# Optimization experiments

Hardware: AMD Instinct MI355X
Metric: run time of the kernel (lower is better)

The kernel has to match this reference:

```python
import jax, jax.numpy as jnp
import numpy as np

FRAME_RATE = 2048
B, T, L = 64, 256, 65536


def setup_inputs() -> dict:
    key = jax.random.key(0)
    ks = jax.random.split(key, 20)
    F = FRAME_RATE
    s = 0.05
    return {
        "alpha": jnp.sort(jax.random.randint(ks[0], (B, T), 0, L), axis=1).astype(jnp.int32),
        "sound": jax.random.normal(ks[1], (B, L), jnp.float32),
        "conv1_w": jax.random.normal(ks[2], (F - 2,), jnp.float32) * s,
        "conv1_b": jax.random.normal(ks[3], (1,), jnp.float32) * s,
        "conv2_w": jax.random.normal(ks[4], (32, 1, 3), jnp.float32) * s,
        "conv2_b": jax.random.normal(ks[5], (32,), jnp.float32) * s,
        "conv3_w": jax.random.normal(ks[6], (128, 32, 3), jnp.float32) * s,
        "conv3_b": jax.random.normal(ks[7], (128,), jnp.float32) * s,
        "lin_w": jax.random.normal(ks[8], (256, 129), jnp.float32) * s,
        "lin_b": jax.random.normal(ks[9], (256,), jnp.float32) * s,
        "w_ih": jax.random.normal(ks[10], (1024, 256), jnp.float32) * s,
        "w_hh": jax.random.normal(ks[11], (1024, 256), jnp.float32) * s,
        "b_ih": jax.random.normal(ks[12], (1024,), jnp.float32) * s,
        "b_hh": jax.random.normal(ks[13], (1024,), jnp.float32) * s,
        "out1_w": jax.random.normal(ks[14], (32, 256), jnp.float32) * s,
        "out1_b": jax.random.normal(ks[15], (32,), jnp.float32) * s,
        "out2_w": jax.random.normal(ks[16], (1, 32), jnp.float32) * s,
        "out2_b": jax.random.normal(ks[17], (1,), jnp.float32) * s,
    }


def reference(alpha, sound, conv1_w, conv1_b, conv2_w, conv2_b, conv3_w, conv3_b,
              lin_w, lin_b, w_ih, w_hh, b_ih, b_hh, out1_w, out1_b, out2_w, out2_b):
    F = conv1_w.shape[0] + 2  # frame_rate
    Bsz, Tlen = alpha.shape
    pad = F // 2
    # Vectorized gather of all per-timestep fragments (replaces nested python loops).
    padded = jnp.pad(sound, ((0, 0), (pad, pad)))               # [B, L + 2*(F//2)]
    idx = alpha[:, :, None] + jnp.arange(F)[None, None, :]      # [B, T, F]
    frags = jnp.take_along_axis(padded[:, None, :], idx, axis=2)  # [B, T, F]
    frags = frags.transpose(1, 0, 2)                            # [T, B, F]
    K = F - 2
    # conv1: 1->1 channel, kernel F-2, output length 3 (three big dot products)
    y1 = jnp.stack([jnp.einsum('tbf,f->tb', frags[:, :, i:i + K], conv1_w)
                    for i in range(3)], axis=-1) + conv1_b[0]   # [T, B, 3]
    # conv2: 1->32 channels, kernel 3, padding 1 (output length stays 3), then ReLU
    y1p = jnp.pad(y1, ((0, 0), (0, 0), (1, 1)))
    win = jnp.stack([y1p[:, :, l:l + 3] for l in range(3)], axis=2)  # [T, B, 3(l), 3(k)]
    y2 = jax.nn.relu(jnp.einsum('tblk,ck->tbcl', win, conv2_w[:, 0, :])
                     + conv2_b[None, None, :, None])            # [T, B, 32, 3]
    # conv3: 32->128 channels, kernel 3, no padding -> output length 1 (no relu, matching source)
    y3 = jnp.einsum('tbck,ock->tbo', y2, conv3_w) + conv3_b     # [T, B, 128]
    # interval = alpha_t - alpha_{t-1} (0 at t=0)
    prev = jnp.concatenate([jnp.zeros((Bsz, 1), alpha.dtype), alpha[:, :-1]], axis=1)
    interval = (alpha - prev).T.astype(frags.dtype)             # [T, B]
    x = jnp.concatenate([interval[..., None], y3], axis=-1)     # [T, B, 129]
    x = x @ lin_w.T + lin_b                                     # [T, B, 256]
    H = w_hh.shape[1]

    def step(carry, xt):
        h, c = carry
        g = xt @ w_ih.T + b_ih + h @ w_hh.T + b_hh              # [B, 4H]
        i_, f_, g_, o_ = jnp.split(g, 4, axis=-1)
        c = jax.nn.sigmoid(f_) * c + jax.nn.sigmoid(i_) * jnp.tanh(g_)
        h = jax.nn.sigmoid(o_) * jnp.tanh(c)
        return (h, c), None

    h0 = jnp.zeros((Bsz, H), x.dtype)
    (h, c), _ = jax.lax.scan(step, (h0, h0), x)
    ht = h[None]                                                # [1, B, 256]
    out = jax.nn.sigmoid(jax.nn.relu(ht @ out1_w.T + out1_b) @ out2_w.T + out2_b)
    return out                                                  # [1, B, 1]
```

## Files before the change

kernel.cpp:

```cpp
#include <hip/hip_runtime.h>
#include <math.h>

#define BSZ 64
#define TLEN 256
#define LSND 65536
#define ZSLOTS 144

__device__ __forceinline__ float sigm(float x) { return 1.f / (1.f + __expf(-x)); }
__device__ __forceinline__ float tanh_f(float x) {
  float e = __expf(-2.f * fabsf(x));
  return copysignf((1.f - e) / (1.f + e), x);
}
__device__ __forceinline__ int zslot(int k) { return (k / 33) * 36 + (k % 33); }

__global__ __launch_bounds__(256) void prep_kernel(
    const float* __restrict__ w_ih, const float* __restrict__ lin_w,
    const float* __restrict__ lin_b, const float* __restrict__ b_ih,
    const float* __restrict__ b_hh, float* __restrict__ Wc, float* __restrict__ bc)
{
  __shared__ float sRow[256];
  const int n = blockIdx.x;
  const int j = threadIdx.x;
  sRow[j] = w_ih[n * 256 + j];
  __syncthreads();
  if (j < 132) {
    float acc = 0.f;
    if (j < 129) {
      for (int k = 0; k < 256; ++k) acc += sRow[k] * lin_w[k * 129 + j];
    }
    Wc[n * 132 + j] = acc;
  } else if (j == 255) {
    float acc = b_ih[n] + b_hh[n];
    for (int k = 0; k < 256; ++k) acc += sRow[k] * lin_b[k];
    bc[n] = acc;
  }
}

__global__ __launch_bounds__(256) void transpose_w3(const float* __restrict__ w3,
                                                    float* __restrict__ w3t)
{
  int i = blockIdx.x * 256 + threadIdx.x;
  if (i < 96 * 128) { int s = i >> 7, o = i & 127; w3t[i] = w3[o * 96 + s]; }
}

__global__ __launch_bounds__(64) void conv_kernel(
    const int* __restrict__ alpha, const float* __restrict__ sound,
    const float* __restrict__ w1, const float* __restrict__ b1v,
    const float* __restrict__ w2, const float* __restrict__ b2,
    const float* __restrict__ w3t, const float* __restrict__ b3,
    float* __restrict__ z)
{
  __shared__ float win[2048];
  __shared__ float sY2[96];
  const int l = threadIdx.x;
  const int b = blockIdx.x >> 8;
  const int t = blockIdx.x & 255;
  const int a = alpha[b * TLEN + t];
  const int a0 = a - 1024;
  const float* srow = sound + (size_t)b * LSND;
  for (int x = l; x < 2048; x += 64) {
    int p = a0 + x;
    win[x] = (p >= 0 && p < LSND) ? srow[p] : 0.f;
  }
  __syncthreads();
  float acc0 = 0.f, acc1 = 0.f, acc2 = 0.f;
  for (int f = l; f < 2046; f += 64) {
    float wv = w1[f];
    acc0 += win[f] * wv;
    acc1 += win[f + 1] * wv;
    acc2 += win[f + 2] * wv;
  }
  for (int m = 32; m; m >>= 1) {
    acc0 += __shfl_xor(acc0, m);
    acc1 += __shfl_xor(acc1, m);
    acc2 += __shfl_xor(acc2, m);
  }
  const float bb = b1v[0];
  const float y11 = acc0 + bb, y12 = acc1 + bb, y13 = acc2 + bb;
  {
    int s = l;
    int c = s / 3, lp = s - c * 3;
    float wA = w2[c * 3], wB = w2[c * 3 + 1], wC = w2[c * 3 + 2];
    float v = (lp == 0) ? (y11 * wB + y12 * wC)
            : (lp == 1) ? (y11 * wA + y12 * wB + y13 * wC)
                        : (y12 * wA + y13 * wB);
    sY2[s] = fmaxf(v + b2[c], 0.f);
    if (l < 32) {
      s = 64 + l; c = s / 3; lp = s - c * 3;
      wA = w2[c * 3]; wB = w2[c * 3 + 1]; wC = w2[c * 3 + 2];
      v = (lp == 0) ? (y11 * wB + y12 * wC)
        : (lp == 1) ? (y11 * wA + y12 * wB + y13 * wC)
                    : (y12 * wA + y13 * wB);
      sY2[s] = fmaxf(v + b2[c], 0.f);
    }
  }
  __syncthreads();
  float o0 = b3[l], o1 = b3[l + 64];
  for (int s = 0; s < 96; ++s) {
    float yv = sY2[s];
    o0 += yv * w3t[s * 128 + l];
    o1 += yv * w3t[s * 128 + l + 64];
  }
  float* zrow = z + ((size_t)t * BSZ + b) * ZSLOTS;
  zrow[zslot(1 + l)] = o0;
  zrow[zslot(65 + l)] = o1;
  if (l == 0) {
    int prev = (t > 0) ? alpha[b * TLEN + t - 1] : 0;
    zrow[0] = (float)(a - prev);
  }
  if (l < 15) {
    int s = (l < 9) ? ((l / 3) * 36 + 33 + (l % 3)) : (138 + (l - 9));
    zrow[s] = 0.f;
  }
}

__global__ void __launch_bounds__(256, 1) lstm_kernel(
    const float* __restrict__ z, const float* __restrict__ Wc,
    const float* __restrict__ bc, const float* __restrict__ w_hh,
    unsigned long long* __restrict__ hbuf, float* __restrict__ hfin)
{
  __shared__ float sH[4][408];
  __shared__ float sP[64][20];
  __shared__ float sG[256];
  __shared__ float sBC[64];

  const int tid = threadIdx.x;
  const int btile = (int)blockIdx.x >> 4;
  const int jt    = (int)blockIdx.x & 15;
  const int w  = tid >> 6;
  const int nl = tid & 63;
  const int ng = ((nl >> 4) << 8) + (jt << 4) + (nl & 15);

  float4 wh[16];
  #pragma unroll
  for (int i = 0; i < 16; ++i)
    wh[i] = *(const float4*)&w_hh[ng * 256 + (w << 6) + (i << 2)];
  float4 wz[9];
  #pragma unroll
  for (int i = 0; i < 9; ++i) {
    float c0 = (i * 4 + 0 < 33) ? Wc[ng * 132 + w * 33 + i * 4 + 0] : 0.f;
    float c1 = (i * 4 + 1 < 33) ? Wc[ng * 132 + w * 33 + i * 4 + 1] : 0.f;
    float c2 = (i * 4 + 2 < 33) ? Wc[ng * 132 + w * 33 + i * 4 + 2] : 0.f;
    float c3 = (i * 4 + 3 < 33) ? Wc[ng * 132 + w * 33 + i * 4 + 3] : 0.f;
    wz[i] = make_float4(c0, c1, c2, c3);
  }
  if (tid < 64) sBC[tid] = bc[((tid >> 4) << 8) + (jt << 4) + (tid & 15)];

  const int zb = (tid < 144) ? tid / 36 : 0;
  const int zc4 = (tid < 144) ? (tid - zb * 36) << 2 : 0;
  float4 zpre = make_float4(0.f, 0.f, 0.f, 0.f);
  if (tid < 144) {
    *(float4*)&sH[zb][256 + zc4] =
        *(const float4*)&z[((size_t)0 * BSZ + (btile << 2) + zb) * ZSLOTS + zc4];
    zpre = *(const float4*)&z[((size_t)1 * BSZ + (btile << 2) + zb) * ZSLOTS + zc4];
  }
  float c_reg = 0.f;
  __syncthreads();

  const int pb = tid & 3;
  const int pjp = (tid & 63) >> 2;
  const int pbase = ((((btile << 2) + pb) << 8) | (w << 6) | pjp);

  for (int t = 0; t < TLEN; ++t) {
    {
      const unsigned long long* hsrc = hbuf + ((size_t)(t & 1) << 14);
      const unsigned tagw = (unsigned)t;
      int rem = 15;
      while (rem) {
        #pragma unroll
        for (int s = 0; s < 4; ++s) {
          if (rem & (1 << s)) {
            unsigned long long v = __hip_atomic_load(hsrc + pbase + (s << 4),
                __ATOMIC_RELAXED, __HIP_MEMORY_SCOPE_AGENT);
            if ((unsigned)v == tagw) {
              sH[pb][(w << 6) | (pjp + (s << 4))] = __uint_as_float((unsigned)(v >> 32));
              rem &= ~(1 << s);
            }
          }
        }
      }
    }
    float a0 = 0.f, a1 = 0.f, a2 = 0.f, a3 = 0.f;
    const int hb = w << 6;
    #pragma unroll
    for (int i = 0; i < 16; ++i) {
      const float4 wv = wh[i];
      float4 h;
      h = *(const float4*)&sH[0][hb + (i << 2)]; a0 += wv.x*h.x + wv.y*h.y + wv.z*h.z + wv.w*h.w;
      h = *(const float4*)&sH[1][hb + (i << 2)]; a1 += wv.x*h.x + wv.y*h.y + wv.z*h.z + wv.w*h.w;
      h = *(const float4*)&sH[2][hb + (i << 2)]; a2 += wv.x*h.x + wv.y*h.y + wv.z*h.z + wv.w*h.w;
      h = *(const float4*)&sH[3][hb + (i << 2)]; a3 += wv.x*h.x + wv.y*h.y + wv.z*h.z + wv.w*h.w;
    }
    const int zbase = 256 + w * 36;
    #pragma unroll
    for (int i = 0; i < 9; ++i) {
      const float4 wv = wz[i];
      float4 v;
      v = *(const float4*)&sH[0][zbase + (i << 2)]; a0 += wv.x*v.x + wv.y*v.y + wv.z*v.z + wv.w*v.w;
      v = *(const float4*)&sH[1][zbase + (i << 2)]; a1 += wv.x*v.x + wv.y*v.y + wv.z*v.z + wv.w*v.w;
      v = *(const float4*)&sH[2][zbase + (i << 2)]; a2 += wv.x*v.x + wv.y*v.y + wv.z*v.z + wv.w*v.w;
      v = *(const float4*)&sH[3][zbase + (i << 2)]; a3 += wv.x*v.x + wv.y*v.y + wv.z*v.z + wv.w*v.w;
    }
    sP[nl][0 + w] = a0;
    sP[nl][4 + w] = a1;
    sP[nl][8 + w] = a2;
    sP[nl][12 + w] = a3;
    __syncthreads();
    {
      const int rn = tid >> 2, rb = tid & 3;
      const float4 p = *(const float4*)&sP[rn][rb << 2];
      sG[tid] = p.x + p.y + p.z + p.w + sBC[rn];
    }
    if (t + 1 < TLEN && tid < 144)
      *(float4*)&sH[zb][256 + zc4] = zpre;
    __syncthreads();
    if (tid < 64) {
      float gi = sG[tid];
      float gf = sG[64 + tid];
      float gg = sG[128 + tid];
      float go = sG[192 + tid];
      c_reg = sigm(gf) * c_reg + sigm(gi) * tanh_f(gg);
      float hv = sigm(go) * tanh_f(c_reg);
      const int jl = tid >> 2, bb = tid & 3;
      const int widx = ((((btile << 2) + bb) << 8) | ((jt << 4) + jl));
      unsigned long long pk =
          ((unsigned long long)__float_as_uint(hv) << 32) | (unsigned)(t + 1);
      __hip_atomic_store(hbuf + (((size_t)((t + 1) & 1)) << 14) + widx, pk,
                         __ATOMIC_RELAXED, __HIP_MEMORY_SCOPE_AGENT);
      if (t == TLEN - 1) hfin[widx] = hv;
    }
    if (t + 2 < TLEN && tid < 144)
      zpre = *(const float4*)&z[((size_t)(t + 2) * BSZ + (btile << 2) + zb) * ZSLOTS + zc4];
  }
}

__global__ __launch_bounds__(256) void head_kernel(
    const float* __restrict__ hfin, const float* __restrict__ o1w,
    const float* __restrict__ o1b, const float* __restrict__ o2w,
    const float* __restrict__ o2b, float* __restrict__ out)
{
  __shared__ float sR[32];
  const int b = blockIdx.x;
  const int tid = threadIdx.x;
  const int m = tid >> 3, g = tid & 7;
  const float* h = hfin + b * 256;
  float acc = 0.f;
  for (int k = g * 32; k < g * 32 + 32; ++k) acc += h[k] * o1w[m * 256 + k];
  acc += __shfl_xor(acc, 1); acc += __shfl_xor(acc, 2); acc += __shfl_xor(acc, 4);
  if (g == 0) sR[m] = fmaxf(acc + o1b[m], 0.f);
  __syncthreads();
  if (tid == 0) {
    float s = o2b[0];
    for (int mm = 0; mm < 32; ++mm) s += sR[mm] * o2w[mm];
    out[b] = sigm(s);
  }
}

extern "C" void kernel_launch(void* const* d_in, const int* in_sizes, int n_in,
                              void* d_out, int out_size, void* d_ws, size_t ws_size,
                              hipStream_t stream) {
  (void)in_sizes; (void)n_in; (void)out_size; (void)ws_size;
  const int*   alpha = (const int*)  d_in[0];
  const float* sound = (const float*)d_in[1];
  const float* w1    = (const float*)d_in[2];
  const float* b1    = (const float*)d_in[3];
  const float* w2    = (const float*)d_in[4];
  const float* b2    = (const float*)d_in[5];
  const float* w3    = (const float*)d_in[6];
  const float* b3    = (const float*)d_in[7];
  const float* linw  = (const float*)d_in[8];
  const float* linb  = (const float*)d_in[9];
  const float* wih   = (const float*)d_in[10];
  const float* whh   = (const float*)d_in[11];
  const float* bih   = (const float*)d_in[12];
  const float* bhh   = (const float*)d_in[13];
  const float* o1w   = (const float*)d_in[14];
  const float* o1b   = (const float*)d_in[15];
  const float* o2w   = (const float*)d_in[16];
  const float* o2b   = (const float*)d_in[17];

  float* z    = (float*)d_ws;
  float* Wc   = z + 2359296;
  float* bc   = Wc + 135168;
  float* w3t  = bc + 1024;
  float* hfin = w3t + 12288;
  unsigned long long* hbuf =
      (unsigned long long*)(hfin + 16384);

  hipMemsetAsync(hbuf, 0, 32768 * 8, stream);

  prep_kernel<<<1024, 256, 0, stream>>>(wih, linw, linb, bih, bhh, Wc, bc);
  transpose_w3<<<48, 256, 0, stream>>>(w3, w3t);
  conv_kernel<<<BSZ * TLEN, 64, 0, stream>>>(alpha, sound, w1, b1, w2, b2, w3t, b3, z);
  lstm_kernel<<<256, 256, 0, stream>>>(z, Wc, bc, whh, hbuf, hfin);
  head_kernel<<<BSZ, 256, 0, stream>>>(hfin, o1w, o1b, o2w, o2b, (float*)d_out);
}
```

Measured before the change: 1.105 ms.

## Run LSTM recurrence on bf16 MFMA with tagged triple-buffered hidden-state exchange

Rewrites the persistent LSTM kernel to compute gate pre-activations with bf16 16x16x32 MFMA. The weights stay in registers as bf16 fragments, and the z inputs are stored as bf16, with the interval split into hi and lo parts to keep its precision. It uses 64 blocks instead of 256 and replaces per-element tagged 64-bit hidden-state words with packed bf16 h values, a triple buffer and per-block tag flags, which cuts global polling traffic and inter-block synchronisation per step. The cost is lower precision in the recurrent matmul across 256 steps, plus a more delicate memory-ordering scheme that relies on s_waitcnt before the tag store.

```diff
diff --git a/kernel.cpp b/kernel.cpp
--- a/kernel.cpp
+++ b/kernel.cpp
@@ -4,14 +4,22 @@
 #define BSZ 64
 #define TLEN 256
 #define LSND 65536
-#define ZSLOTS 144
+#define ZK 160
+
+typedef __attribute__((ext_vector_type(8))) short bf16x8;
+typedef __attribute__((ext_vector_type(4))) float f32x4;
 
 __device__ __forceinline__ float sigm(float x) { return 1.f / (1.f + __expf(-x)); }
 __device__ __forceinline__ float tanh_f(float x) {
   float e = __expf(-2.f * fabsf(x));
   return copysignf((1.f - e) / (1.f + e), x);
 }
-__device__ __forceinline__ int zslot(int k) { return (k / 33) * 36 + (k % 33); }
+__device__ __forceinline__ unsigned short f2bf(float x) {
+  unsigned u = __float_as_uint(x);
+  return (unsigned short)((u + 0x7FFFu + ((u >> 16) & 1u)) >> 16);
+}
+
+union U16x8 { ulonglong2 u2; bf16x8 v; };
 
 __global__ __launch_bounds__(256) void prep_kernel(
     const float* __restrict__ w_ih, const float* __restrict__ lin_w,
@@ -48,7 +56,7 @@
     const float* __restrict__ w1, const float* __restrict__ b1v,
     const float* __restrict__ w2, const float* __restrict__ b2,
     const float* __restrict__ w3t, const float* __restrict__ b3,
-    float* __restrict__ z)
+    unsigned short* __restrict__ zw)
 {
   __shared__ float win[2048];
   __shared__ float sY2[96];
@@ -101,137 +109,156 @@
     o0 += yv * w3t[s * 128 + l];
     o1 += yv * w3t[s * 128 + l + 64];
   }
-  float* zrow = z + ((size_t)t * BSZ + b) * ZSLOTS;
-  zrow[zslot(1 + l)] = o0;
-  zrow[zslot(65 + l)] = o1;
+  unsigned short* zrow = zw + ((size_t)t * BSZ + b) * ZK;
+  zrow[1 + l] = f2bf(o0);
+  zrow[65 + l] = f2bf(o1);
   if (l == 0) {
     int prev = (t > 0) ? alpha[b * TLEN + t - 1] : 0;
-    zrow[0] = (float)(a - prev);
-  }
-  if (l < 15) {
-    int s = (l < 9) ? ((l / 3) * 36 + 33 + (l % 3)) : (138 + (l - 9));
-    zrow[s] = 0.f;
-  }
+    float iv = (float)(a - prev);
+    unsigned short hi = f2bf(iv);
+    zrow[0] = hi;
+    float rec = __uint_as_float(((unsigned)hi) << 16);
+    zrow[129] = f2bf(iv - rec);
+  }
+  if (l < 30) zrow[130 + l] = 0;
 }
 
 __global__ void __launch_bounds__(256, 1) lstm_kernel(
-    const float* __restrict__ z, const float* __restrict__ Wc,
+    const unsigned short* __restrict__ zw, const float* __restrict__ Wc,
     const float* __restrict__ bc, const float* __restrict__ w_hh,
-    unsigned long long* __restrict__ hbuf, float* __restrict__ hfin)
-{
-  __shared__ float sH[4][408];
-  __shared__ float sP[64][20];
-  __shared__ float sG[256];
-  __shared__ float sBC[64];
+    unsigned short* __restrict__ hpub, unsigned int* __restrict__ tags,
+    float* __restrict__ hfin)
+{
+  __shared__ float sD[2][4][320];
 
   const int tid = threadIdx.x;
-  const int btile = (int)blockIdx.x >> 4;
-  const int jt    = (int)blockIdx.x & 15;
-  const int w  = tid >> 6;
-  const int nl = tid & 63;
-  const int ng = ((nl >> 4) << 8) + (jt << 4) + (nl & 15);
-
-  float4 wh[16];
-  #pragma unroll
-  for (int i = 0; i < 16; ++i)
-    wh[i] = *(const float4*)&w_hh[ng * 256 + (w << 6) + (i << 2)];
-  float4 wz[9];
-  #pragma unroll
-  for (int i = 0; i < 9; ++i) {
-    float c0 = (i * 4 + 0 < 33) ? Wc[ng * 132 + w * 33 + i * 4 + 0] : 0.f;
-    float c1 = (i * 4 + 1 < 33) ? Wc[ng * 132 + w * 33 + i * 4 + 1] : 0.f;
-    float c2 = (i * 4 + 2 < 33) ? Wc[ng * 132 + w * 33 + i * 4 + 2] : 0.f;
-    float c3 = (i * 4 + 3 < 33) ? Wc[ng * 132 + w * 33 + i * 4 + 3] : 0.f;
-    wz[i] = make_float4(c0, c1, c2, c3);
-  }
-  if (tid < 64) sBC[tid] = bc[((tid >> 4) << 8) + (jt << 4) + (tid & 15)];
-
-  const int zb = (tid < 144) ? tid / 36 : 0;
-  const int zc4 = (tid < 144) ? (tid - zb * 36) << 2 : 0;
-  float4 zpre = make_float4(0.f, 0.f, 0.f, 0.f);
-  if (tid < 144) {
-    *(float4*)&sH[zb][256 + zc4] =
-        *(const float4*)&z[((size_t)0 * BSZ + (btile << 2) + zb) * ZSLOTS + zc4];
-    zpre = *(const float4*)&z[((size_t)1 * BSZ + (btile << 2) + zb) * ZSLOTS + zc4];
-  }
-  float c_reg = 0.f;
-  __syncthreads();
-
-  const int pb = tid & 3;
-  const int pjp = (tid & 63) >> 2;
-  const int pbase = ((((btile << 2) + pb) << 8) | (w << 6) | pjp);
-
-  for (int t = 0; t < TLEN; ++t) {
-    {
-      const unsigned long long* hsrc = hbuf + ((size_t)(t & 1) << 14);
-      const unsigned tagw = (unsigned)t;
-      int rem = 15;
-      while (rem) {
-        #pragma unroll
-        for (int s = 0; s < 4; ++s) {
-          if (rem & (1 << s)) {
-            unsigned long long v = __hip_atomic_load(hsrc + pbase + (s << 4),
-                __ATOMIC_RELAXED, __HIP_MEMORY_SCOPE_AGENT);
-            if ((unsigned)v == tagw) {
-              sH[pb][(w << 6) | (pjp + (s << 4))] = __uint_as_float((unsigned)(v >> 32));
-              rem &= ~(1 << s);
-            }
-          }
+  const int wv = tid >> 6;
+  const int ln = tid & 63;
+  const int jt = (int)blockIdx.x >> 2;
+  const int bt = (int)blockIdx.x & 3;
+  const int bl = ln & 15;
+  const int kg = ln >> 4;
+  const int b = (bt << 4) + bl;
+
+  bf16x8 afr[13];
+  {
+    const int row = (wv << 8) + (jt << 4) + bl;
+    #pragma unroll
+    for (int o = 0; o < 13; ++o) {
+      #pragma unroll
+      for (int e = 0; e < 8; ++e) {
+        int k = o * 32 + kg * 8 + e;
+        float w;
+        if (k < 256) w = w_hh[row * 256 + k];
+        else {
+          int kz = k - 256;
+          w = (kz < 129) ? Wc[row * 132 + kz] : (kz == 129 ? Wc[row * 132] : 0.f);
         }
+        afr[o][e] = (short)f2bf(w);
       }
     }
-    float a0 = 0.f, a1 = 0.f, a2 = 0.f, a3 = 0.f;
-    const int hb = w << 6;
-    #pragma unroll
-    for (int i = 0; i < 16; ++i) {
-      const float4 wv = wh[i];
-      float4 h;
-      h = *(const float4*)&sH[0][hb + (i << 2)]; a0 += wv.x*h.x + wv.y*h.y + wv.z*h.z + wv.w*h.w;
-      h = *(const float4*)&sH[1][hb + (i << 2)]; a1 += wv.x*h.x + wv.y*h.y + wv.z*h.z + wv.w*h.w;
-      h = *(const float4*)&sH[2][hb + (i << 2)]; a2 += wv.x*h.x + wv.y*h.y + wv.z*h.z + wv.w*h.w;
-      h = *(const float4*)&sH[3][hb + (i << 2)]; a3 += wv.x*h.x + wv.y*h.y + wv.z*h.z + wv.w*h.w;
-    }
-    const int zbase = 256 + w * 36;
-    #pragma unroll
-    for (int i = 0; i < 9; ++i) {
-      const float4 wv = wz[i];
-      float4 v;
-      v = *(const float4*)&sH[0][zbase + (i << 2)]; a0 += wv.x*v.x + wv.y*v.y + wv.z*v.z + wv.w*v.w;
-      v = *(const float4*)&sH[1][zbase + (i << 2)]; a1 += wv.x*v.x + wv.y*v.y + wv.z*v.z + wv.w*v.w;
-      v = *(const float4*)&sH[2][zbase + (i << 2)]; a2 += wv.x*v.x + wv.y*v.y + wv.z*v.z + wv.w*v.w;
-      v = *(const float4*)&sH[3][zbase + (i << 2)]; a3 += wv.x*v.x + wv.y*v.y + wv.z*v.z + wv.w*v.w;
-    }
-    sP[nl][0 + w] = a0;
-    sP[nl][4 + w] = a1;
-    sP[nl][8 + w] = a2;
-    sP[nl][12 + w] = a3;
-    __syncthreads();
-    {
-      const int rn = tid >> 2, rb = tid & 3;
-      const float4 p = *(const float4*)&sP[rn][rb << 2];
-      sG[tid] = p.x + p.y + p.z + p.w + sBC[rn];
-    }
-    if (t + 1 < TLEN && tid < 144)
-      *(float4*)&sH[zb][256 + zc4] = zpre;
-    __syncthreads();
-    if (tid < 64) {
-      float gi = sG[tid];
-      float gf = sG[64 + tid];
-      float gg = sG[128 + tid];
-      float go = sG[192 + tid];
-      c_reg = sigm(gf) * c_reg + sigm(gi) * tanh_f(gg);
-      float hv = sigm(go) * tanh_f(c_reg);
-      const int jl = tid >> 2, bb = tid & 3;
-      const int widx = ((((btile << 2) + bb) << 8) | ((jt << 4) + jl));
-      unsigned long long pk =
-          ((unsigned long long)__float_as_uint(hv) << 32) | (unsigned)(t + 1);
-      __hip_atomic_store(hbuf + (((size_t)((t + 1) & 1)) << 14) + widx, pk,
-                         __ATOMIC_RELAXED, __HIP_MEMORY_SCOPE_AGENT);
-      if (t == TLEN - 1) hfin[widx] = hv;
-    }
-    if (t + 2 < TLEN && tid < 144)
-      zpre = *(const float4*)&z[((size_t)(t + 2) * BSZ + (btile << 2) + zb) * ZSLOTS + zc4];
-  }
+  }
+  float bias[4];
+  #pragma unroll
+  for (int r = 0; r < 4; ++r)
+    bias[r] = bc[(wv << 8) + (jt << 4) + (kg << 2) + r];
+
+  const unsigned long long* hp64 = (const unsigned long long*)hpub;
+  unsigned* hp32 = (unsigned*)hpub;
+
+  ulonglong2 zA[5], zB[5];
+  #pragma unroll
+  for (int oz = 0; oz < 5; ++oz) {
+    zA[oz] = *(const ulonglong2*)(zw + (((size_t)0 * BSZ + b) * ZK + oz * 32 + kg * 8));
+    zB[oz] = *(const ulonglong2*)(zw + (((size_t)1 * BSZ + b) * ZK + oz * 32 + kg * 8));
+  }
+  float c0 = 0.f, c1 = 0.f, c2 = 0.f, c3 = 0.f;
+
+#define STEP(T, SDP, BUF, NBUF, ZC)                                             \
+  {                                                                             \
+    const int t_ = (T);                                                         \
+    f32x4 acc; acc[0] = bias[0]; acc[1] = bias[1]; acc[2] = bias[2]; acc[3] = bias[3]; \
+    _Pragma("unroll")                                                           \
+    for (int oz = 0; oz < 5; ++oz) {                                            \
+      U16x8 u; u.u2 = ZC[oz];                                                   \
+      acc = __builtin_amdgcn_mfma_f32_16x16x32_bf16(afr[8 + oz], u.v, acc, 0, 0, 0); \
+    }                                                                           \
+    if (ln < 16) {                                                              \
+      const unsigned* tp = tags + (BUF) * 64 + (bt << 4) + ln;                  \
+      unsigned v;                                                               \
+      do { v = __hip_atomic_load(tp, __ATOMIC_RELAXED, __HIP_MEMORY_SCOPE_AGENT); } \
+      while (v != (unsigned)t_);                                                \
+    }                                                                           \
+    _Pragma("unroll")                                                           \
+    for (int o = 0; o < 8; ++o) {                                               \
+      const unsigned long long* hp = hp64 + (size_t)(BUF) * 4096 + b * 64 + o * 8 + kg * 2; \
+      U16x8 u;                                                                  \
+      u.u2.x = __hip_atomic_load(hp,     __ATOMIC_RELAXED, __HIP_MEMORY_SCOPE_AGENT); \
+      u.u2.y = __hip_atomic_load(hp + 1, __ATOMIC_RELAXED, __HIP_MEMORY_SCOPE_AGENT); \
+      acc = __builtin_amdgcn_mfma_f32_16x16x32_bf16(afr[o], u.v, acc, 0, 0, 0); \
+    }                                                                           \
+    sD[SDP][wv][ln * 5 + 0] = acc[0];                                           \
+    sD[SDP][wv][ln * 5 + 1] = acc[1];                                           \
+    sD[SDP][wv][ln * 5 + 2] = acc[2];                                           \
+    sD[SDP][wv][ln * 5 + 3] = acc[3];                                           \
+    __syncthreads();                                                            \
+    if (wv == 0) {                                                              \
+      float hv0, hv1, hv2, hv3;                                                 \
+      {                                                                         \
+        float gi = sD[SDP][0][ln * 5 + 0], gf = sD[SDP][1][ln * 5 + 0];         \
+        float gg = sD[SDP][2][ln * 5 + 0], go = sD[SDP][3][ln * 5 + 0];         \
+        c0 = sigm(gf) * c0 + sigm(gi) * tanh_f(gg); hv0 = sigm(go) * tanh_f(c0); \
+      }                                                                         \
+      {                                                                         \
+        float gi = sD[SDP][0][ln * 5 + 1], gf = sD[SDP][1][ln * 5 + 1];         \
+        float gg = sD[SDP][2][ln * 5 + 1], go = sD[SDP][3][ln * 5 + 1];         \
+        c1 = sigm(gf) * c1 + sigm(gi) * tanh_f(gg); hv1 = sigm(go) * tanh_f(c1); \
+      }                                                                         \
+      {                                                                         \
+        float gi = sD[SDP][0][ln * 5 + 2], gf = sD[SDP][1][ln * 5 + 2];         \
+        float gg = sD[SDP][2][ln * 5 + 2], go = sD[SDP][3][ln * 5 + 2];         \
+        c2 = sigm(gf) * c2 + sigm(gi) * tanh_f(gg); hv2 = sigm(go) * tanh_f(c2); \
+      }                                                                         \
+      {                                                                         \
+        float gi = sD[SDP][0][ln * 5 + 3], gf = sD[SDP][1][ln * 5 + 3];         \
+        float gg = sD[SDP][2][ln * 5 + 3], go = sD[SDP][3][ln * 5 + 3];         \
+        c3 = sigm(gf) * c3 + sigm(gi) * tanh_f(gg); hv3 = sigm(go) * tanh_f(c3); \
+      }                                                                         \
+      unsigned p0 = (unsigned)f2bf(hv0) | ((unsigned)f2bf(hv1) << 16);          \
+      unsigned p1 = (unsigned)f2bf(hv2) | ((unsigned)f2bf(hv3) << 16);          \
+      unsigned* hq = hp32 + (size_t)(NBUF) * 8192 + b * 128 + (jt << 3) + (kg << 1); \
+      __hip_atomic_store(hq,     p0, __ATOMIC_RELAXED, __HIP_MEMORY_SCOPE_AGENT); \
+      __hip_atomic_store(hq + 1, p1, __ATOMIC_RELAXED, __HIP_MEMORY_SCOPE_AGENT); \
+      if (t_ == TLEN - 1) {                                                     \
+        const int j0 = (jt << 4) + (kg << 2);                                   \
+        hfin[b * 256 + j0 + 0] = hv0;                                           \
+        hfin[b * 256 + j0 + 1] = hv1;                                           \
+        hfin[b * 256 + j0 + 2] = hv2;                                           \
+        hfin[b * 256 + j0 + 3] = hv3;                                           \
+      }                                                                         \
+      asm volatile("s_waitcnt vmcnt(0)" ::: "memory");                          \
+      if (ln == 0)                                                              \
+        __hip_atomic_store(tags + (NBUF) * 64 + (bt << 4) + jt,                 \
+                           (unsigned)(t_ + 1), __ATOMIC_RELAXED,                \
+                           __HIP_MEMORY_SCOPE_AGENT);                           \
+    }                                                                           \
+    if (t_ + 2 < TLEN) {                                                        \
+      _Pragma("unroll")                                                         \
+      for (int oz = 0; oz < 5; ++oz)                                            \
+        ZC[oz] = *(const ulonglong2*)(zw + (((size_t)(t_ + 2) * BSZ + b) * ZK + oz * 32 + kg * 8)); \
+    }                                                                           \
+  }
+
+  int buf = 0;
+  #pragma unroll 1
+  for (int t = 0; t < TLEN; t += 2) {
+    int n1 = buf + 1; if (n1 == 3) n1 = 0;
+    int n2 = n1 + 1; if (n2 == 3) n2 = 0;
+    STEP(t,     0, buf, n1, zA)
+    STEP(t + 1, 1, n1,  n2, zB)
+    buf = n2;
+  }
+#undef STEP
 }
 
 __global__ __launch_bounds__(256) void head_kernel(
@@ -279,19 +306,20 @@
   const float* o2w   = (const float*)d_in[16];
   const float* o2b   = (const float*)d_in[17];
 
-  float* z    = (float*)d_ws;
-  float* Wc   = z + 2359296;
-  float* bc   = Wc + 135168;
-  float* w3t  = bc + 1024;
-  float* hfin = w3t + 12288;
-  unsigned long long* hbuf =
-      (unsigned long long*)(hfin + 16384);
-
-  hipMemsetAsync(hbuf, 0, 32768 * 8, stream);
+  char* p = (char*)d_ws;
+  unsigned short* zw   = (unsigned short*)p;
+  float*          Wc   = (float*)(p + 5242880);
+  float*          bc   = (float*)(p + 5783552);
+  float*          w3t  = (float*)(p + 5787648);
+  float*          hfin = (float*)(p + 5836800);
+  unsigned short* hpub = (unsigned short*)(p + 5902336);
+  unsigned int*   tags = (unsigned int*)(p + 6000640);
+
+  hipMemsetAsync(p + 5902336, 0, 98304 + 768, stream);
 
   prep_kernel<<<1024, 256, 0, stream>>>(wih, linw, linb, bih, bhh, Wc, bc);
   transpose_w3<<<48, 256, 0, stream>>>(w3, w3t);
-  conv_kernel<<<BSZ * TLEN, 64, 0, stream>>>(alpha, sound, w1, b1, w2, b2, w3t, b3, z);
-  lstm_kernel<<<256, 256, 0, stream>>>(z, Wc, bc, whh, hbuf, hfin);
+  conv_kernel<<<BSZ * TLEN, 64, 0, stream>>>(alpha, sound, w1, b1, w2, b2, w3t, b3, zw);
+  lstm_kernel<<<64, 256, 0, stream>>>(zw, Wc, bc, whh, hpub, tags, hfin);
   head_kernel<<<BSZ, 256, 0, stream>>>(hfin, o1w, o1b, o2w, o2b, (float*)d_out);
 }
```

Result: slower. 1.311 ms (+18.7%).
